# Optimization experiments

Measured on AMD Instinct MI355X. Metric: run time of the kernel, lower is better.

The kernel has to match this reference:

```python
import jax, jax.numpy as jnp
import numpy as np

B, N, S, D, K = 8, 8192, 2048, 256, 3
MLP = [256, 128]
EPS = 1e-5


def setup_inputs() -> dict:
    key = jax.random.key(0)
    ks = jax.random.split(key, 12)
    inp = {
        "xyz1": jax.random.normal(ks[0], (B, N, 3), dtype=jnp.float32),
        "xyz2": jax.random.normal(ks[1], (B, S, 3), dtype=jnp.float32),
        "points1": jax.random.normal(ks[2], (B, N, D), dtype=jnp.float32),
        "points2": jax.random.normal(ks[3], (B, S, D), dtype=jnp.float32),
        # relation conv: Conv2d(4 -> 1, kernel 1x1) == linear over last dim
        "rel_w": jax.random.normal(ks[4], (4,), dtype=jnp.float32) * 0.5,
        "rel_b": jnp.zeros((), dtype=jnp.float32),
        # mlp layer 0: Conv1d(2D -> 256, k=1) + BN
        "W0": jax.random.normal(ks[5], (MLP[0], 2 * D), dtype=jnp.float32) * (1.0 / np.sqrt(2 * D)),
        "b0": jnp.zeros((MLP[0],), dtype=jnp.float32),
        "g0": jnp.ones((MLP[0],), dtype=jnp.float32),
        "be0": jnp.zeros((MLP[0],), dtype=jnp.float32),
        # mlp layer 1: Conv1d(256 -> 128, k=1) + BN
        "W1": jax.random.normal(ks[6], (MLP[1], MLP[0]), dtype=jnp.float32) * (1.0 / np.sqrt(MLP[0])),
        "b1": jnp.zeros((MLP[1],), dtype=jnp.float32),
        "g1": jnp.ones((MLP[1],), dtype=jnp.float32),
        "be1": jnp.zeros((MLP[1],), dtype=jnp.float32),
    }
    return inp


def _gather(points, idx):
    # points: [B,S,C], idx: [B,N,K] -> [B,N,K,C]
    return jax.vmap(lambda p, i: p[i])(points, idx)


def _bn_relu(x, gamma, beta):
    # training-mode BatchNorm1d over [B,N,C]: stats over (B,N), biased var
    mean = jnp.mean(x, axis=(0, 1))
    var = jnp.var(x, axis=(0, 1))
    xn = (x - mean) * jax.lax.rsqrt(var + EPS)
    return jax.nn.relu(xn * gamma + beta)


def reference(xyz1, xyz2, points1, points2, rel_w, rel_b,
              W0, b0, g0, be0, W1, b1, g1, be1):
    # pairwise squared distances [B,N,S]
    d = (jnp.sum(xyz1 ** 2, -1)[:, :, None]
         + jnp.sum(xyz2 ** 2, -1)[:, None, :]
         - 2.0 * jnp.einsum('bnc,bmc->bnm', xyz1, xyz2))
    neg_d, idx = jax.lax.top_k(-d, K)          # K smallest distances
    dists = -neg_d                              # [B,N,K]

    offset = xyz1[:, :, None, :] - _gather(xyz2, idx)        # [B,N,K,3]
    rel = jnp.concatenate([dists[..., None], offset], -1)    # [B,N,K,4]
    weight = jax.nn.sigmoid(rel @ rel_w + rel_b)              # [B,N,K]

    interp = jnp.mean(_gather(points2, idx) * weight[..., None], axis=2)  # [B,N,D]
    h = jnp.concatenate([points1, interp], axis=-1)           # [B,N,2D]

    h = _bn_relu(jnp.einsum('bnc,oc->bno', h, W0) + b0, g0, be0)
    h = _bn_relu(jnp.einsum('bnc,oc->bno', h, W1) + b1, g1, be1)
    return h  # [B,N,128]
```

## Files before the change

kernel.cpp:

```cpp
#include <hip/hip_runtime.h>
#include <stdint.h>
#include <stddef.h>

#define B_   8
#define N_   8192
#define S_   2048
#define D_   256
#define M_   (B_*N_)
#define C0_  256
#define C1_  128
#define K2D_ 512
#define TS8_ 8
#define SEG8_ (S_/TS8_)

typedef __attribute__((ext_vector_type(8))) short short8;
typedef __attribute__((ext_vector_type(4))) short short4v;
typedef __attribute__((ext_vector_type(4))) float f32x4;
typedef __attribute__((ext_vector_type(2))) float f32x2;

__device__ __forceinline__ short f2bf(float f) {
  unsigned u = __float_as_uint(f);
  u += 0x7fffu + ((u >> 16) & 1u);
  return (short)(u >> 16);
}
__device__ __forceinline__ float bf2f(short s) {
  return __uint_as_float(((unsigned)(unsigned short)s) << 16);
}

__device__ __forceinline__ void cp16(const void* g, void* l) {
  __builtin_amdgcn_global_load_lds(
      (__attribute__((address_space(1))) void*)(g),
      (__attribute__((address_space(3))) void*)(l), 16, 0, 0);
}

__global__ void convw_kernel(const float* __restrict__ W0,
                             const float* __restrict__ W1,
                             const float* __restrict__ xyz2,
                             short* __restrict__ W0b, short* __restrict__ W1b,
                             float* __restrict__ xyz2p, float* __restrict__ stats) {
  int i = blockIdx.x * 256 + threadIdx.x;
  if (blockIdx.x == 0) {
    stats[threadIdx.x] = 0.f;
    stats[256 + threadIdx.x] = 0.f;
    stats[512 + threadIdx.x] = 0.f;
  }
  if (i < C0_ * K2D_) W0b[i] = f2bf(W0[i]);
  if (i < C1_ * C0_)  W1b[i] = f2bf(W1[i]);
  if (i < B_ * S_) {
    const int b = i >> 11, s = i & (S_ - 1);
    float x = xyz2[(size_t)i * 3 + 0];
    float y = xyz2[(size_t)i * 3 + 1];
    float z = xyz2[(size_t)i * 3 + 2];
    float ss = __fadd_rn(__fadd_rn(__fmul_rn(x, x), __fmul_rn(y, y)), __fmul_rn(z, z));
    float* xw = xyz2p + (size_t)b * 4 * S_;
    xw[s] = x; xw[S_ + s] = y; xw[2 * S_ + s] = z; xw[3 * S_ + s] = ss;
  }
}

__global__ __launch_bounds__(512, 8)
void topk_kernel(const float* __restrict__ xyz1, const float* __restrict__ xyz2p,
                 const float* __restrict__ relw, const float* __restrict__ relb,
                 int* __restrict__ idx_out, float* __restrict__ w_out) {
  __shared__ float cd[TS8_][64][3];
  __shared__ int   ci[TS8_][64][3];
  const int tid  = threadIdx.x;
  const int lane = tid & 63;
  const int seg  = __builtin_amdgcn_readfirstlane(tid >> 6);
  const int b    = blockIdx.x >> 7;
  const int n    = (blockIdx.x & 127) * 64 + lane;

  const float* p = xyz1 + ((size_t)b * N_ + n) * 3;
  const float ax = p[0], ay = p[1], az = p[2];
  const float s1 = __fadd_rn(__fadd_rn(__fmul_rn(ax, ax), __fmul_rn(ay, ay)), __fmul_rn(az, az));

  const float* xw = xyz2p + (size_t)b * 4 * S_;
  const f32x2* XP = (const f32x2*)(xw)           + seg * (SEG8_ / 2);
  const f32x2* YP = (const f32x2*)(xw + S_)      + seg * (SEG8_ / 2);
  const f32x2* ZP = (const f32x2*)(xw + 2 * S_)  + seg * (SEG8_ / 2);
  const f32x2* WP = (const f32x2*)(xw + 3 * S_)  + seg * (SEG8_ / 2);

  float d0 = 3.4e38f, d1 = 3.4e38f, d2 = 3.4e38f;
  int   i0 = 0, i1 = 0, i2 = 0;
  const int sbeg = seg * SEG8_;
  {
    #pragma clang fp contract(off)
    #pragma unroll 4
    for (int pr = 0; pr < SEG8_ / 2; pr++) {
      f32x2 X = XP[pr], Y = YP[pr], Z = ZP[pr], W = WP[pr];
      f32x2 t1 = ax * X;
      f32x2 t2 = ay * Y;
      f32x2 t3 = az * Z;
      f32x2 dt = (t1 + t2) + t3;
      f32x2 e  = s1 + W;
      f32x2 m  = 2.0f * dt;
      f32x2 d  = e - m;
      const float dlo = d.x, dhi = d.y;
      if (fminf(dlo, dhi) < d2) {
        const int s = sbeg + 2 * pr;
        if (dlo < d2) {
          if (dlo < d1) {
            d2 = d1; i2 = i1;
            if (dlo < d0) { d1 = d0; i1 = i0; d0 = dlo; i0 = s; }
            else          { d1 = dlo; i1 = s; }
          } else { d2 = dlo; i2 = s; }
        }
        if (dhi < d2) {
          if (dhi < d1) {
            d2 = d1; i2 = i1;
            if (dhi < d0) { d1 = d0; i1 = i0; d0 = dhi; i0 = s + 1; }
            else          { d1 = dhi; i1 = s + 1; }
          } else { d2 = dhi; i2 = s + 1; }
        }
      }
    }
  }
  cd[seg][lane][0] = d0; cd[seg][lane][1] = d1; cd[seg][lane][2] = d2;
  ci[seg][lane][0] = i0; ci[seg][lane][1] = i1; ci[seg][lane][2] = i2;
  __syncthreads();

  if (tid < 64) {
    float m0 = 3.4e38f, m1 = 3.4e38f, m2 = 3.4e38f;
    int   j0 = 0, j1 = 0, j2 = 0;
    #pragma unroll
    for (int sg = 0; sg < TS8_; sg++) {
      #pragma unroll
      for (int k = 0; k < 3; k++) {
        float d = cd[sg][tid][k];
        int   ix = ci[sg][tid][k];
        if (d < m2) {
          if (d < m1) {
            m2 = m1; j2 = j1;
            if (d < m0) { m1 = m0; j1 = j0; m0 = d; j0 = ix; }
            else        { m1 = d;  j1 = ix; }
          } else { m2 = d; j2 = ix; }
        }
      }
    }
    const float w0r = relw[0], w1r = relw[1], w2r = relw[2], w3r = relw[3], br = relb[0];
    const size_t base = ((size_t)b * N_ + n) * 3;
    float dd[3] = {m0, m1, m2};
    int   ii[3] = {j0, j1, j2};
    #pragma unroll
    for (int k = 0; k < 3; k++) {
      const int s = ii[k];
      float ox = ax - xw[s], oy = ay - xw[S_ + s], oz = az - xw[2 * S_ + s];
      float t = dd[k] * w0r + ox * w1r + oy * w2r + oz * w3r + br;
      float w = 1.0f / (1.0f + expf(-t));
      idx_out[base + k] = s;
      w_out[base + k] = w * (1.0f / 3.0f);
    }
  }
}

__global__ __launch_bounds__(256, 3)
void gemm1_kernel(const float* __restrict__ p1, const float* __restrict__ p2,
                  const int* __restrict__ idx, const float* __restrict__ wts,
                  const short* __restrict__ Bw, const float* __restrict__ bias,
                  short* __restrict__ Cb, float* __restrict__ stats) {
  __shared__ __align__(16) short sA[128 * 32];
  __shared__ __align__(16) short sB[128 * 32];
  const int tid = threadIdx.x;
  const int lane = tid & 63;
  const int wave = tid >> 6;
  const int wm = wave & 1;
  const int wn = wave >> 1;
  const size_t mbase = (size_t)blockIdx.x * 128;
  const int nbase = blockIdx.y * 128;
  const int lrow = lane >> 2;
  const int lcol = (lane & 3) * 8;

  f32x4 acc[4][4] = {};

  for (int k0 = 0; k0 < K2D_; k0 += 32) {
    #pragma unroll
    for (int t = 0; t < 2; t++) {
      const int r = wave * 32 + t * 16;
      const int row = (int)mbase + r + lrow;
      cp16(Bw + (size_t)(nbase + r + lrow) * K2D_ + k0 + lcol, &sB[r * 32]);
      float v[8];
      if (k0 < D_) {
        const float* src = p1 + (size_t)row * D_ + k0 + lcol;
        float4 f0 = *(const float4*)src;
        float4 f1 = *(const float4*)(src + 4);
        v[0] = f0.x; v[1] = f0.y; v[2] = f0.z; v[3] = f0.w;
        v[4] = f1.x; v[5] = f1.y; v[6] = f1.z; v[7] = f1.w;
      } else {
        const int c2 = k0 - D_ + lcol;
        const int bb = row >> 13;
        const float* pb = p2 + (size_t)bb * S_ * D_;
        const int i0 = idx[row * 3 + 0], i1 = idx[row * 3 + 1], i2 = idx[row * 3 + 2];
        const float w0 = wts[row * 3 + 0], w1 = wts[row * 3 + 1], w2 = wts[row * 3 + 2];
        const float* q0 = pb + (size_t)i0 * D_ + c2;
        const float* q1 = pb + (size_t)i1 * D_ + c2;
        const float* q2 = pb + (size_t)i2 * D_ + c2;
        float4 a0 = *(const float4*)q0, a1v = *(const float4*)(q0 + 4);
        float4 b0 = *(const float4*)q1, b1v = *(const float4*)(q1 + 4);
        float4 c0 = *(const float4*)q2, c1v = *(const float4*)(q2 + 4);
        v[0] = w0 * a0.x + w1 * b0.x + w2 * c0.x;
        v[1] = w0 * a0.y + w1 * b0.y + w2 * c0.y;
        v[2] = w0 * a0.z + w1 * b0.z + w2 * c0.z;
        v[3] = w0 * a0.w + w1 * b0.w + w2 * c0.w;
        v[4] = w0 * a1v.x + w1 * b1v.x + w2 * c1v.x;
        v[5] = w0 * a1v.y + w1 * b1v.y + w2 * c1v.y;
        v[6] = w0 * a1v.z + w1 * b1v.z + w2 * c1v.z;
        v[7] = w0 * a1v.w + w1 * b1v.w + w2 * c1v.w;
      }
      short8 o;
      #pragma unroll
      for (int e = 0; e < 8; e++) o[e] = f2bf(v[e]);
      *(short8*)&sA[(r + lrow) * 32 + lcol] = o;
    }
    __syncthreads();

    const int mr = lane & 15;
    const int ks = (lane >> 4) * 8;
    short8 af[4], bfr[4];
    #pragma unroll
    for (int i = 0; i < 4; i++) af[i]  = *(const short8*)&sA[(wm * 64 + i * 16 + mr) * 32 + ks];
    #pragma unroll
    for (int j = 0; j < 4; j++) bfr[j] = *(const short8*)&sB[(wn * 64 + j * 16 + mr) * 32 + ks];
    #pragma unroll
    for (int i = 0; i < 4; i++)
      #pragma unroll
      for (int j = 0; j < 4; j++)
        acc[i][j] = __builtin_amdgcn_mfma_f32_16x16x32_bf16(af[i], bfr[j], acc[i][j], 0, 0, 0);
    __syncthreads();
  }

  const int cr = (lane >> 4) * 4;
  const int cc = lane & 15;
  float ps[4], ps2[4];
  #pragma unroll
  for (int j = 0; j < 4; j++) {
    const int col = nbase + wn * 64 + j * 16 + cc;
    const float bv = bias[col];
    float s = 0.f, s2 = 0.f;
    #pragma unroll
    for (int i = 0; i < 4; i++) {
      #pragma unroll
      for (int r = 0; r < 4; r++) {
        const float v = acc[i][j][r];
        s += v; s2 += v * v;
        const size_t row = mbase + wm * 64 + i * 16 + cr + r;
        Cb[row * C0_ + col] = f2bf(v + bv);
      }
    }
    ps[j] = s; ps2[j] = s2;
  }
  #pragma unroll
  for (int j = 0; j < 4; j++) {
    ps[j]  += __shfl_xor(ps[j], 16);  ps[j]  += __shfl_xor(ps[j], 32);
    ps2[j] += __shfl_xor(ps2[j], 16); ps2[j] += __shfl_xor(ps2[j], 32);
  }
  float* sred = (float*)sA;
  if (wm == 1 && lane < 16) {
    #pragma unroll
    for (int j = 0; j < 4; j++) {
      const int c = wn * 64 + j * 16 + lane;
      sred[2 * c] = ps[j]; sred[2 * c + 1] = ps2[j];
    }
  }
  __syncthreads();
  if (wm == 0 && lane < 16) {
    #pragma unroll
    for (int j = 0; j < 4; j++) {
      const int c = wn * 64 + j * 16 + lane;
      atomicAdd(&stats[nbase + c],       ps[j]  + sred[2 * c]);
      atomicAdd(&stats[C0_ + nbase + c], ps2[j] + sred[2 * c + 1]);
    }
  }
}

__global__ __launch_bounds__(256, 2)
void gemm2_kernel(const short* __restrict__ A, const short* __restrict__ Bw,
                  const float* __restrict__ ssn, const float* __restrict__ bias,
                  short* __restrict__ Cb, float* __restrict__ stats) {
  __shared__ __align__(16) short sA[128 * 32];
  __shared__ __align__(16) short sB[128 * 32];
  const int tid = threadIdx.x;
  const int lane = tid & 63;
  const int wave = tid >> 6;
  const int wm = wave & 1;
  const int wn = wave >> 1;
  const size_t mbase = (size_t)blockIdx.x * 128;
  const int lrow = lane >> 2;
  const int lcol = (lane & 3) * 8;

  f32x4 acc[4][4] = {};

  for (int k0 = 0; k0 < C0_; k0 += 32) {
    float4 sca = *(const float4*)(ssn + k0 + lcol);
    float4 scb = *(const float4*)(ssn + k0 + lcol + 4);
    float4 sha = *(const float4*)(ssn + C0_ + k0 + lcol);
    float4 shb = *(const float4*)(ssn + C0_ + k0 + lcol + 4);
    #pragma unroll
    for (int t = 0; t < 2; t++) {
      const int r = wave * 32 + t * 16;
      const int row = (int)mbase + r + lrow;
      cp16(Bw + (size_t)(r + lrow) * C0_ + k0 + lcol, &sB[r * 32]);
      short8 av = *(const short8*)(A + (size_t)row * C0_ + k0 + lcol);
      float sc[8] = {sca.x, sca.y, sca.z, sca.w, scb.x, scb.y, scb.z, scb.w};
      float sh[8] = {sha.x, sha.y, sha.z, sha.w, shb.x, shb.y, shb.z, shb.w};
      short8 o;
      #pragma unroll
      for (int e = 0; e < 8; e++) {
        float v = bf2f(av[e]) * sc[e] + sh[e];
        o[e] = f2bf(v > 0.f ? v : 0.f);
      }
      *(short8*)&sA[(r + lrow) * 32 + lcol] = o;
    }
    __syncthreads();

    const int mr = lane & 15;
    const int ks = (lane >> 4) * 8;
    short8 af[4], bfr[4];
    #pragma unroll
    for (int i = 0; i < 4; i++) af[i]  = *(const short8*)&sA[(wm * 64 + i * 16 + mr) * 32 + ks];
    #pragma unroll
    for (int j = 0; j < 4; j++) bfr[j] = *(const short8*)&sB[(wn * 64 + j * 16 + mr) * 32 + ks];
    #pragma unroll
    for (int i = 0; i < 4; i++)
      #pragma unroll
      for (int j = 0; j < 4; j++)
        acc[i][j] = __builtin_amdgcn_mfma_f32_16x16x32_bf16(af[i], bfr[j], acc[i][j], 0, 0, 0);
    __syncthreads();
  }

  const int cr = (lane >> 4) * 4;
  const int cc = lane & 15;
  float ps[4], ps2[4];
  #pragma unroll
  for (int j = 0; j < 4; j++) {
    const int col = wn * 64 + j * 16 + cc;
    const float bv = bias[col];
    float s = 0.f, s2 = 0.f;
    #pragma unroll
    for (int i = 0; i < 4; i++) {
      #pragma unroll
      for (int r = 0; r < 4; r++) {
        const float v = acc[i][j][r];
        s += v; s2 += v * v;
        const size_t row = mbase + wm * 64 + i * 16 + cr + r;
        Cb[row * C1_ + col] = f2bf(v + bv);
      }
    }
    ps[j] = s; ps2[j] = s2;
  }
  #pragma unroll
  for (int j = 0; j < 4; j++) {
    ps[j]  += __shfl_xor(ps[j], 16);  ps[j]  += __shfl_xor(ps[j], 32);
    ps2[j] += __shfl_xor(ps2[j], 16); ps2[j] += __shfl_xor(ps2[j], 32);
  }
  float* sred = (float*)sA;
  if (wm == 1 && lane < 16) {
    #pragma unroll
    for (int j = 0; j < 4; j++) {
      const int c = wn * 64 + j * 16 + lane;
      sred[2 * c] = ps[j]; sred[2 * c + 1] = ps2[j];
    }
  }
  __syncthreads();
  if (wm == 0 && lane < 16) {
    #pragma unroll
    for (int j = 0; j < 4; j++) {
      const int c = wn * 64 + j * 16 + lane;
      atomicAdd(&stats[c],       ps[j]  + sred[2 * c]);
      atomicAdd(&stats[C1_ + c], ps2[j] + sred[2 * c + 1]);
    }
  }
}

__global__ void stats_final_kernel(const float* __restrict__ stats, const int C,
                                   const float* __restrict__ bias,
                                   const float* __restrict__ g, const float* __restrict__ be,
                                   float* __restrict__ ss) {
  const int c = threadIdx.x;
  if (c >= C) return;
  const float inv = 1.0f / (float)M_;
  float m0 = stats[c] * inv;
  float var = stats[C + c] * inv - m0 * m0;
  float mean = m0 + bias[c];
  float sc = g[c] * rsqrtf(var + 1e-5f);
  ss[c] = sc;
  ss[C + c] = be[c] - mean * sc;
}

__global__ __launch_bounds__(256, 1)
void norm2_kernel(const short* __restrict__ a2, const float* __restrict__ ss,
                  float* __restrict__ out) {
  const size_t t = (size_t)blockIdx.x * 256 + threadIdx.x;
  const size_t base = t * 8;
  const int c = (int)(base & (C1_ - 1));
  short8 v8 = *(const short8*)(a2 + base);
  float vv[8];
  #pragma unroll
  for (int k = 0; k < 8; k++) {
    float v = bf2f(v8[k]) * ss[c + k] + ss[C1_ + c + k];
    vv[k] = v > 0.f ? v : 0.f;
  }
  *(float4*)(out + base)     = make_float4(vv[0], vv[1], vv[2], vv[3]);
  *(float4*)(out + base + 4) = make_float4(vv[4], vv[5], vv[6], vv[7]);
}

extern "C" void kernel_launch(void* const* d_in, const int* in_sizes, int n_in,
                              void* d_out, int out_size, void* d_ws, size_t ws_size,
                              hipStream_t stream) {
  const float* xyz1 = (const float*)d_in[0];
  const float* xyz2 = (const float*)d_in[1];
  const float* pts1 = (const float*)d_in[2];
  const float* pts2 = (const float*)d_in[3];
  const float* relw = (const float*)d_in[4];
  const float* relb = (const float*)d_in[5];
  const float* W0   = (const float*)d_in[6];
  const float* b0   = (const float*)d_in[7];
  const float* g0   = (const float*)d_in[8];
  const float* be0  = (const float*)d_in[9];
  const float* W1   = (const float*)d_in[10];
  const float* b1   = (const float*)d_in[11];
  const float* g1   = (const float*)d_in[12];
  const float* be1  = (const float*)d_in[13];

  char* ws = (char*)d_ws;
  constexpr size_t IDX_OFF = 0;
  constexpr size_t WTS_OFF = IDX_OFF + (size_t)M_ * 3 * 4;
  constexpr size_t W0B_OFF = WTS_OFF + (size_t)M_ * 3 * 4;
  constexpr size_t W1B_OFF = W0B_OFF + (size_t)C0_ * K2D_ * 2;
  constexpr size_t XW_OFF  = W1B_OFF + (size_t)C1_ * C0_ * 2;
  constexpr size_t A1_OFF  = XW_OFF + (size_t)B_ * 4 * S_ * 4;
  constexpr size_t A2_OFF  = A1_OFF + (size_t)M_ * C0_ * 2;
  constexpr size_t ST_OFF  = A2_OFF + (size_t)M_ * C1_ * 2;
  constexpr size_t SS1_OFF = ST_OFF + (size_t)768 * 4;
  constexpr size_t SS2_OFF = SS1_OFF + (size_t)2 * C0_ * 4;

  int*   idx   = (int*)(ws + IDX_OFF);
  float* wts   = (float*)(ws + WTS_OFF);
  short* W0b   = (short*)(ws + W0B_OFF);
  short* W1b   = (short*)(ws + W1B_OFF);
  float* xyz2p = (float*)(ws + XW_OFF);
  short* a1    = (short*)(ws + A1_OFF);
  short* a2    = (short*)(ws + A2_OFF);
  float* st    = (float*)(ws + ST_OFF);
  float* ss1   = (float*)(ws + SS1_OFF);
  float* ss2   = (float*)(ws + SS2_OFF);
  float* outp  = (float*)d_out;

  convw_kernel<<<512, 256, 0, stream>>>(W0, W1, xyz2, W0b, W1b, xyz2p, st);
  topk_kernel<<<B_ * (N_ / 64), 512, 0, stream>>>(xyz1, xyz2p, relw, relb, idx, wts);

  gemm1_kernel<<<dim3(M_ / 128, C0_ / 128), 256, 0, stream>>>(
      pts1, pts2, idx, wts, W0b, b0, a1, st);
  stats_final_kernel<<<1, 256, 0, stream>>>(st, C0_, b0, g0, be0, ss1);

  gemm2_kernel<<<dim3(M_ / 128, 1), 256, 0, stream>>>(a1, W1b, ss1, b1, a2, st + 512);
  stats_final_kernel<<<1, 128, 0, stream>>>(st + 512, C1_, b1, g1, be1, ss2);
  norm2_kernel<<<(size_t)M_ * C1_ / 8 / 256, 256, 0, stream>>>(a2, ss2, outp);
}
```

Before: 306.0 us.

## Widen gemm1 tile to full N with double-buffered B and preload W1 in gemm2

gemm1 now computes all 256 output channels per block instead of splitting them over two blocks. This removes the duplicated gather and interpolation of the A operand (points1 and the 3-NN weighted points2). It also double-buffers the weight tile in LDS and prefetches the next A registers during the MFMA loop. gemm2 loads the entire W1 matrix into padded LDS once and lets each wave read its own A rows directly from global, dropping the per-step A staging and syncs. The costs are higher register pressure (32 accumulators per wave in gemm1), lower occupancy bounds, and more LDS use.

```diff
diff --git a/kernel.cpp b/kernel.cpp
--- a/kernel.cpp
+++ b/kernel.cpp
@@ -12,9 +12,9 @@
 #define K2D_ 512
 #define TS8_ 8
 #define SEG8_ (S_/TS8_)
+#define SWP_ 264
 
 typedef __attribute__((ext_vector_type(8))) short short8;
-typedef __attribute__((ext_vector_type(4))) short short4v;
 typedef __attribute__((ext_vector_type(4))) float f32x4;
 typedef __attribute__((ext_vector_type(2))) float f32x2;
 
@@ -152,131 +152,13 @@
   }
 }
 
-__global__ __launch_bounds__(256, 3)
+__global__ __launch_bounds__(256, 2)
 void gemm1_kernel(const float* __restrict__ p1, const float* __restrict__ p2,
                   const int* __restrict__ idx, const float* __restrict__ wts,
                   const short* __restrict__ Bw, const float* __restrict__ bias,
                   short* __restrict__ Cb, float* __restrict__ stats) {
   __shared__ __align__(16) short sA[128 * 32];
-  __shared__ __align__(16) short sB[128 * 32];
-  const int tid = threadIdx.x;
-  const int lane = tid & 63;
-  const int wave = tid >> 6;
-  const int wm = wave & 1;
-  const int wn = wave >> 1;
-  const size_t mbase = (size_t)blockIdx.x * 128;
-  const int nbase = blockIdx.y * 128;
-  const int lrow = lane >> 2;
-  const int lcol = (lane & 3) * 8;
-
-  f32x4 acc[4][4] = {};
-
-  for (int k0 = 0; k0 < K2D_; k0 += 32) {
-    #pragma unroll
-    for (int t = 0; t < 2; t++) {
-      const int r = wave * 32 + t * 16;
-      const int row = (int)mbase + r + lrow;
-      cp16(Bw + (size_t)(nbase + r + lrow) * K2D_ + k0 + lcol, &sB[r * 32]);
-      float v[8];
-      if (k0 < D_) {
-        const float* src = p1 + (size_t)row * D_ + k0 + lcol;
-        float4 f0 = *(const float4*)src;
-        float4 f1 = *(const float4*)(src + 4);
-        v[0] = f0.x; v[1] = f0.y; v[2] = f0.z; v[3] = f0.w;
-        v[4] = f1.x; v[5] = f1.y; v[6] = f1.z; v[7] = f1.w;
-      } else {
-        const int c2 = k0 - D_ + lcol;
-        const int bb = row >> 13;
-        const float* pb = p2 + (size_t)bb * S_ * D_;
-        const int i0 = idx[row * 3 + 0], i1 = idx[row * 3 + 1], i2 = idx[row * 3 + 2];
-        const float w0 = wts[row * 3 + 0], w1 = wts[row * 3 + 1], w2 = wts[row * 3 + 2];
-        const float* q0 = pb + (size_t)i0 * D_ + c2;
-        const float* q1 = pb + (size_t)i1 * D_ + c2;
-        const float* q2 = pb + (size_t)i2 * D_ + c2;
-        float4 a0 = *(const float4*)q0, a1v = *(const float4*)(q0 + 4);
-        float4 b0 = *(const float4*)q1, b1v = *(const float4*)(q1 + 4);
-        float4 c0 = *(const float4*)q2, c1v = *(const float4*)(q2 + 4);
-        v[0] = w0 * a0.x + w1 * b0.x + w2 * c0.x;
-        v[1] = w0 * a0.y + w1 * b0.y + w2 * c0.y;
-        v[2] = w0 * a0.z + w1 * b0.z + w2 * c0.z;
-        v[3] = w0 * a0.w + w1 * b0.w + w2 * c0.w;
-        v[4] = w0 * a1v.x + w1 * b1v.x + w2 * c1v.x;
-        v[5] = w0 * a1v.y + w1 * b1v.y + w2 * c1v.y;
-        v[6] = w0 * a1v.z + w1 * b1v.z + w2 * c1v.z;
-        v[7] = w0 * a1v.w + w1 * b1v.w + w2 * c1v.w;
-      }
-      short8 o;
-      #pragma unroll
-      for (int e = 0; e < 8; e++) o[e] = f2bf(v[e]);
-      *(short8*)&sA[(r + lrow) * 32 + lcol] = o;
-    }
-    __syncthreads();
-
-    const int mr = lane & 15;
-    const int ks = (lane >> 4) * 8;
-    short8 af[4], bfr[4];
-    #pragma unroll
-    for (int i = 0; i < 4; i++) af[i]  = *(const short8*)&sA[(wm * 64 + i * 16 + mr) * 32 + ks];
-    #pragma unroll
-    for (int j = 0; j < 4; j++) bfr[j] = *(const short8*)&sB[(wn * 64 + j * 16 + mr) * 32 + ks];
-    #pragma unroll
-    for (int i = 0; i < 4; i++)
-      #pragma unroll
-      for (int j = 0; j < 4; j++)
-        acc[i][j] = __builtin_amdgcn_mfma_f32_16x16x32_bf16(af[i], bfr[j], acc[i][j], 0, 0, 0);
-    __syncthreads();
-  }
-
-  const int cr = (lane >> 4) * 4;
-  const int cc = lane & 15;
-  float ps[4], ps2[4];
-  #pragma unroll
-  for (int j = 0; j < 4; j++) {
-    const int col = nbase + wn * 64 + j * 16 + cc;
-    const float bv = bias[col];
-    float s = 0.f, s2 = 0.f;
-    #pragma unroll
-    for (int i = 0; i < 4; i++) {
-      #pragma unroll
-      for (int r = 0; r < 4; r++) {
-        const float v = acc[i][j][r];
-        s += v; s2 += v * v;
-        const size_t row = mbase + wm * 64 + i * 16 + cr + r;
-        Cb[row * C0_ + col] = f2bf(v + bv);
-      }
-    }
-    ps[j] = s; ps2[j] = s2;
-  }
-  #pragma unroll
-  for (int j = 0; j < 4; j++) {
-    ps[j]  += __shfl_xor(ps[j], 16);  ps[j]  += __shfl_xor(ps[j], 32);
-    ps2[j] += __shfl_xor(ps2[j], 16); ps2[j] += __shfl_xor(ps2[j], 32);
-  }
-  float* sred = (float*)sA;
-  if (wm == 1 && lane < 16) {
-    #pragma unroll
-    for (int j = 0; j < 4; j++) {
-      const int c = wn * 64 + j * 16 + lane;
-      sred[2 * c] = ps[j]; sred[2 * c + 1] = ps2[j];
-    }
-  }
-  __syncthreads();
-  if (wm == 0 && lane < 16) {
-    #pragma unroll
-    for (int j = 0; j < 4; j++) {
-      const int c = wn * 64 + j * 16 + lane;
-      atomicAdd(&stats[nbase + c],       ps[j]  + sred[2 * c]);
-      atomicAdd(&stats[C0_ + nbase + c], ps2[j] + sred[2 * c + 1]);
-    }
-  }
-}
-
-__global__ __launch_bounds__(256, 2)
-void gemm2_kernel(const short* __restrict__ A, const short* __restrict__ Bw,
-                  const float* __restrict__ ssn, const float* __restrict__ bias,
-                  short* __restrict__ Cb, float* __restrict__ stats) {
-  __shared__ __align__(16) short sA[128 * 32];
-  __shared__ __align__(16) short sB[128 * 32];
+  __shared__ __align__(16) short sB[2][256 * 32];
   const int tid = threadIdx.x;
   const int lane = tid & 63;
   const int wave = tid >> 6;
@@ -286,86 +168,238 @@
   const int lrow = lane >> 2;
   const int lcol = (lane & 3) * 8;
 
-  f32x4 acc[4][4] = {};
-
-  for (int k0 = 0; k0 < C0_; k0 += 32) {
-    float4 sca = *(const float4*)(ssn + k0 + lcol);
-    float4 scb = *(const float4*)(ssn + k0 + lcol + 4);
-    float4 sha = *(const float4*)(ssn + C0_ + k0 + lcol);
-    float4 shb = *(const float4*)(ssn + C0_ + k0 + lcol + 4);
+  int rowg[2]; int ia[2][3]; float wa[2][3]; const float* pbase[2];
+  #pragma unroll
+  for (int t = 0; t < 2; t++) {
+    const int row = (int)mbase + wave * 32 + t * 16 + lrow;
+    rowg[t] = row;
+    pbase[t] = p2 + (size_t)(row >> 13) * S_ * D_;
+    ia[t][0] = idx[row * 3 + 0]; ia[t][1] = idx[row * 3 + 1]; ia[t][2] = idx[row * 3 + 2];
+    wa[t][0] = wts[row * 3 + 0]; wa[t][1] = wts[row * 3 + 1]; wa[t][2] = wts[row * 3 + 2];
+  }
+
+  f32x4 acc[4][8] = {};
+  float4 v[2][6];
+
+  #define LOAD_A(K0)                                                          \
+    if ((K0) < D_) {                                                          \
+      _Pragma("unroll")                                                       \
+      for (int t = 0; t < 2; t++) {                                           \
+        const float* src = p1 + (size_t)rowg[t] * D_ + (K0) + lcol;           \
+        v[t][0] = *(const float4*)src; v[t][1] = *(const float4*)(src + 4);   \
+      }                                                                       \
+    } else {                                                                  \
+      const int c2 = (K0) - D_ + lcol;                                        \
+      _Pragma("unroll")                                                       \
+      for (int t = 0; t < 2; t++) {                                           \
+        const float* q0 = pbase[t] + (size_t)ia[t][0] * D_ + c2;              \
+        const float* q1 = pbase[t] + (size_t)ia[t][1] * D_ + c2;              \
+        const float* q2 = pbase[t] + (size_t)ia[t][2] * D_ + c2;              \
+        v[t][0] = *(const float4*)q0; v[t][1] = *(const float4*)(q0 + 4);     \
+        v[t][2] = *(const float4*)q1; v[t][3] = *(const float4*)(q1 + 4);     \
+        v[t][4] = *(const float4*)q2; v[t][5] = *(const float4*)(q2 + 4);     \
+      }                                                                       \
+    }
+
+  #define STAGE_B(K0, BUF)                                                    \
+    _Pragma("unroll")                                                         \
+    for (int t = 0; t < 4; t++) {                                             \
+      const int r = wave * 64 + t * 16;                                       \
+      cp16(Bw + (size_t)(r + lrow) * K2D_ + (K0) + lcol, &sB[BUF][r * 32]);   \
+    }
+
+  LOAD_A(0);
+  STAGE_B(0, 0);
+
+  for (int k0 = 0, it = 0; k0 < K2D_; k0 += 32, it++) {
     #pragma unroll
     for (int t = 0; t < 2; t++) {
       const int r = wave * 32 + t * 16;
-      const int row = (int)mbase + r + lrow;
-      cp16(Bw + (size_t)(r + lrow) * C0_ + k0 + lcol, &sB[r * 32]);
-      short8 av = *(const short8*)(A + (size_t)row * C0_ + k0 + lcol);
-      float sc[8] = {sca.x, sca.y, sca.z, sca.w, scb.x, scb.y, scb.z, scb.w};
-      float sh[8] = {sha.x, sha.y, sha.z, sha.w, shb.x, shb.y, shb.z, shb.w};
+      float fv[8];
+      if (k0 < D_) {
+        fv[0] = v[t][0].x; fv[1] = v[t][0].y; fv[2] = v[t][0].z; fv[3] = v[t][0].w;
+        fv[4] = v[t][1].x; fv[5] = v[t][1].y; fv[6] = v[t][1].z; fv[7] = v[t][1].w;
+      } else {
+        fv[0] = wa[t][0] * v[t][0].x + wa[t][1] * v[t][2].x + wa[t][2] * v[t][4].x;
+        fv[1] = wa[t][0] * v[t][0].y + wa[t][1] * v[t][2].y + wa[t][2] * v[t][4].y;
+        fv[2] = wa[t][0] * v[t][0].z + wa[t][1] * v[t][2].z + wa[t][2] * v[t][4].z;
+        fv[3] = wa[t][0] * v[t][0].w + wa[t][1] * v[t][2].w + wa[t][2] * v[t][4].w;
+        fv[4] = wa[t][0] * v[t][1].x + wa[t][1] * v[t][3].x + wa[t][2] * v[t][5].x;
+        fv[5] = wa[t][0] * v[t][1].y + wa[t][1] * v[t][3].y + wa[t][2] * v[t][5].y;
+        fv[6] = wa[t][0] * v[t][1].z + wa[t][1] * v[t][3].z + wa[t][2] * v[t][5].z;
+        fv[7] = wa[t][0] * v[t][1].w + wa[t][1] * v[t][3].w + wa[t][2] * v[t][5].w;
+      }
       short8 o;
       #pragma unroll
-      for (int e = 0; e < 8; e++) {
-        float v = bf2f(av[e]) * sc[e] + sh[e];
-        o[e] = f2bf(v > 0.f ? v : 0.f);
-      }
+      for (int e = 0; e < 8; e++) o[e] = f2bf(fv[e]);
       *(short8*)&sA[(r + lrow) * 32 + lcol] = o;
     }
     __syncthreads();
+
+    const int kn = k0 + 32;
+    if (kn < K2D_) {
+      STAGE_B(kn, (it + 1) & 1);
+      LOAD_A(kn);
+    }
 
     const int mr = lane & 15;
     const int ks = (lane >> 4) * 8;
-    short8 af[4], bfr[4];
+    short8 af[4], bfr[8];
     #pragma unroll
     for (int i = 0; i < 4; i++) af[i]  = *(const short8*)&sA[(wm * 64 + i * 16 + mr) * 32 + ks];
     #pragma unroll
-    for (int j = 0; j < 4; j++) bfr[j] = *(const short8*)&sB[(wn * 64 + j * 16 + mr) * 32 + ks];
+    for (int j = 0; j < 8; j++) bfr[j] = *(const short8*)&sB[it & 1][(wn * 128 + j * 16 + mr) * 32 + ks];
     #pragma unroll
     for (int i = 0; i < 4; i++)
       #pragma unroll
-      for (int j = 0; j < 4; j++)
+      for (int j = 0; j < 8; j++)
         acc[i][j] = __builtin_amdgcn_mfma_f32_16x16x32_bf16(af[i], bfr[j], acc[i][j], 0, 0, 0);
     __syncthreads();
   }
+  #undef LOAD_A
+  #undef STAGE_B
 
   const int cr = (lane >> 4) * 4;
   const int cc = lane & 15;
-  float ps[4], ps2[4];
-  #pragma unroll
-  for (int j = 0; j < 4; j++) {
-    const int col = wn * 64 + j * 16 + cc;
+  float ps[8], ps2[8];
+  #pragma unroll
+  for (int j = 0; j < 8; j++) {
+    const int col = wn * 128 + j * 16 + cc;
     const float bv = bias[col];
     float s = 0.f, s2 = 0.f;
     #pragma unroll
     for (int i = 0; i < 4; i++) {
       #pragma unroll
       for (int r = 0; r < 4; r++) {
-        const float v = acc[i][j][r];
-        s += v; s2 += v * v;
+        const float vv = acc[i][j][r];
+        s += vv; s2 += vv * vv;
         const size_t row = mbase + wm * 64 + i * 16 + cr + r;
-        Cb[row * C1_ + col] = f2bf(v + bv);
+        Cb[row * C0_ + col] = f2bf(vv + bv);
       }
     }
     ps[j] = s; ps2[j] = s2;
   }
   #pragma unroll
-  for (int j = 0; j < 4; j++) {
+  for (int j = 0; j < 8; j++) {
     ps[j]  += __shfl_xor(ps[j], 16);  ps[j]  += __shfl_xor(ps[j], 32);
     ps2[j] += __shfl_xor(ps2[j], 16); ps2[j] += __shfl_xor(ps2[j], 32);
   }
   float* sred = (float*)sA;
   if (wm == 1 && lane < 16) {
     #pragma unroll
-    for (int j = 0; j < 4; j++) {
-      const int c = wn * 64 + j * 16 + lane;
+    for (int j = 0; j < 8; j++) {
+      const int c = wn * 128 + j * 16 + lane;
       sred[2 * c] = ps[j]; sred[2 * c + 1] = ps2[j];
     }
   }
   __syncthreads();
   if (wm == 0 && lane < 16) {
     #pragma unroll
-    for (int j = 0; j < 4; j++) {
-      const int c = wn * 64 + j * 16 + lane;
+    for (int j = 0; j < 8; j++) {
+      const int c = wn * 128 + j * 16 + lane;
       atomicAdd(&stats[c],       ps[j]  + sred[2 * c]);
-      atomicAdd(&stats[C1_ + c], ps2[j] + sred[2 * c + 1]);
+      atomicAdd(&stats[C0_ + c], ps2[j] + sred[2 * c + 1]);
+    }
+  }
+}
+
+__global__ __launch_bounds__(256, 2)
+void gemm2_kernel(const short* __restrict__ A, const short* __restrict__ Bw,
+                  const float* __restrict__ ssn, const float* __restrict__ bias,
+                  short* __restrict__ Cb, float* __restrict__ stats) {
+  __shared__ __align__(16) short sW[C1_ * SWP_];
+  __shared__ float sred[3 * 256];
+  const int tid = threadIdx.x;
+  const int lane = tid & 63;
+  const int wave = tid >> 6;
+  const size_t mbase = (size_t)blockIdx.x * 128;
+
+  #pragma unroll
+  for (int i = 0; i < 16; i++) {
+    const int flat = i * 256 + tid;
+    const int n = flat >> 5;
+    const int kb = flat & 31;
+    *(short8*)&sW[n * SWP_ + kb * 8] = *(const short8*)(Bw + (size_t)flat * 8);
+  }
+  __syncthreads();
+
+  f32x4 acc[2][8] = {};
+  const int mr = lane & 15;
+  const int ksq = (lane >> 4) * 8;
+
+  for (int k0 = 0; k0 < C0_; k0 += 32) {
+    const int kk = k0 + ksq;
+    float4 sc0 = *(const float4*)(ssn + kk);
+    float4 sc1 = *(const float4*)(ssn + kk + 4);
+    float4 sh0 = *(const float4*)(ssn + C0_ + kk);
+    float4 sh1 = *(const float4*)(ssn + C0_ + kk + 4);
+    const float sc[8] = {sc0.x, sc0.y, sc0.z, sc0.w, sc1.x, sc1.y, sc1.z, sc1.w};
+    const float sh[8] = {sh0.x, sh0.y, sh0.z, sh0.w, sh1.x, sh1.y, sh1.z, sh1.w};
+    short8 af[2];
+    #pragma unroll
+    for (int i = 0; i < 2; i++) {
+      const size_t row = mbase + wave * 32 + i * 16 + mr;
+      short8 av = *(const short8*)(A + row * C0_ + kk);
+      short8 o;
+      #pragma unroll
+      for (int e = 0; e < 8; e++) {
+        float f = bf2f(av[e]) * sc[e] + sh[e];
+        o[e] = f2bf(f > 0.f ? f : 0.f);
+      }
+      af[i] = o;
+    }
+    short8 bf8[8];
+    #pragma unroll
+    for (int j = 0; j < 8; j++) bf8[j] = *(const short8*)&sW[(j * 16 + mr) * SWP_ + kk];
+    #pragma unroll
+    for (int i = 0; i < 2; i++)
+      #pragma unroll
+      for (int j = 0; j < 8; j++)
+        acc[i][j] = __builtin_amdgcn_mfma_f32_16x16x32_bf16(af[i], bf8[j], acc[i][j], 0, 0, 0);
+  }
+
+  const int cr = (lane >> 4) * 4;
+  const int cc = lane & 15;
+  float ps[8], ps2[8];
+  #pragma unroll
+  for (int j = 0; j < 8; j++) {
+    const int col = j * 16 + cc;
+    const float bv = bias[col];
+    float s = 0.f, s2 = 0.f;
+    #pragma unroll
+    for (int i = 0; i < 2; i++) {
+      #pragma unroll
+      for (int r = 0; r < 4; r++) {
+        const float vv = acc[i][j][r];
+        s += vv; s2 += vv * vv;
+        const size_t row = mbase + wave * 32 + i * 16 + cr + r;
+        Cb[row * C1_ + col] = f2bf(vv + bv);
+      }
+    }
+    ps[j] = s; ps2[j] = s2;
+  }
+  #pragma unroll
+  for (int j = 0; j < 8; j++) {
+    ps[j]  += __shfl_xor(ps[j], 16);  ps[j]  += __shfl_xor(ps[j], 32);
+    ps2[j] += __shfl_xor(ps2[j], 16); ps2[j] += __shfl_xor(ps2[j], 32);
+  }
+  if (wave > 0 && lane < 16) {
+    #pragma unroll
+    for (int j = 0; j < 8; j++) {
+      const int c = j * 16 + lane;
+      sred[(wave - 1) * 256 + c]       = ps[j];
+      sred[(wave - 1) * 256 + 128 + c] = ps2[j];
+    }
+  }
+  __syncthreads();
+  if (wave == 0 && lane < 16) {
+    #pragma unroll
+    for (int j = 0; j < 8; j++) {
+      const int c = j * 16 + lane;
+      float s  = ps[j]  + sred[c]       + sred[256 + c]       + sred[512 + c];
+      float s2 = ps2[j] + sred[128 + c] + sred[256 + 128 + c] + sred[512 + 128 + c];
+      atomicAdd(&stats[c],       s);
+      atomicAdd(&stats[C1_ + c], s2);
     }
   }
 }
@@ -447,11 +481,10 @@
   convw_kernel<<<512, 256, 0, stream>>>(W0, W1, xyz2, W0b, W1b, xyz2p, st);
   topk_kernel<<<B_ * (N_ / 64), 512, 0, stream>>>(xyz1, xyz2p, relw, relb, idx, wts);
 
-  gemm1_kernel<<<dim3(M_ / 128, C0_ / 128), 256, 0, stream>>>(
-      pts1, pts2, idx, wts, W0b, b0, a1, st);
+  gemm1_kernel<<<M_ / 128, 256, 0, stream>>>(pts1, pts2, idx, wts, W0b, b0, a1, st);
   stats_final_kernel<<<1, 256, 0, stream>>>(st, C0_, b0, g0, be0, ss1);
 
-  gemm2_kernel<<<dim3(M_ / 128, 1), 256, 0, stream>>>(a1, W1b, ss1, b1, a2, st + 512);
+  gemm2_kernel<<<M_ / 128, 256, 0, stream>>>(a1, W1b, ss1, b1, a2, st + 512);
   stats_final_kernel<<<1, 128, 0, stream>>>(st + 512, C1_, b1, g1, be1, ss2);
   norm2_kernel<<<(size_t)M_ * C1_ / 8 / 256, 256, 0, stream>>>(a2, ss2, outp);
 }
```

After: 292.1 us. 1.05x faster.
